# Performance work log

Hardware: AMD Instinct MI355X
Metric: run time of the kernel (lower is better)

## Reference

```python
import jax, jax.numpy as jnp
import numpy as np

B, T, D, S, P, R = 8, 512, 256, 64, 1024, 12


def setup_inputs() -> dict:
    key = jax.random.key(0)
    ks = jax.random.split(key, 8)
    encoded = jax.random.normal(ks[0], (B, T, D), dtype=jnp.float32)
    span_starts = jax.random.randint(ks[1], (B, S), 0, 500).astype(jnp.int32)
    span_lens = jax.random.randint(ks[2], (B, S), 0, 12).astype(jnp.int32)  # end = start + len + 1 <= T
    pair_head = jax.random.randint(ks[3], (B, P), 0, S).astype(jnp.int32)
    pair_tail = jax.random.randint(ks[4], (B, P), 0, S).astype(jnp.int32)
    W_linear = (jax.random.normal(ks[5], (2 * D, R), dtype=jnp.float32) / np.sqrt(2 * D)).astype(jnp.float32)
    b_linear = jnp.zeros((R,), dtype=jnp.float32)
    W_bilinear = (jax.random.normal(ks[6], (R, D, D), dtype=jnp.float32) / D).astype(jnp.float32)
    return dict(encoded=encoded, W_linear=W_linear, b_linear=b_linear, W_bilinear=W_bilinear,
                span_starts=span_starts, span_lens=span_lens, pair_head=pair_head, pair_tail=pair_tail)


def reference(encoded, W_linear, b_linear, W_bilinear, span_starts, span_lens, pair_head, pair_tail):
    # --- ragged span max-pooling (self.pool = max over encoded[b, start:end]) ---
    span_ends = span_starts + span_lens + 1  # exclusive end, length >= 1
    pos = jnp.arange(T)  # [T]
    in_span = (pos[None, None, :] >= span_starts[:, :, None]) & (pos[None, None, :] < span_ends[:, :, None])  # [B,S,T]
    neg_inf = jnp.finfo(encoded.dtype).min
    span_pooled = jnp.max(jnp.where(in_span[..., None], encoded[:, None, :, :], neg_inf), axis=2)  # [B,S,D]

    # --- pair feature gather: [span_pooled[head], span_pooled[tail]] ---
    head = jnp.take_along_axis(span_pooled, pair_head[..., None].astype(jnp.int32), axis=1)  # [B,P,D]
    tail = jnp.take_along_axis(span_pooled, pair_tail[..., None].astype(jnp.int32), axis=1)  # [B,P,D]
    pair_rep = jnp.concatenate([head, tail], axis=-1)  # [B,P,2D]

    # --- linear + bilinear classifier, sigmoid scores ---
    scores = pair_rep @ W_linear + b_linear  # [B,P,R]
    scores = scores + jnp.einsum('bpd,rde,bpe->bpr', head, W_bilinear, tail)
    return jax.nn.sigmoid(scores)
```

## Files before the change

### kernel.cpp

```cpp
#include <hip/hip_runtime.h>
#include <math.h>

#define B 8
#define T 512
#define D 256
#define S 64
#define P 1024
#define R 12

typedef __attribute__((ext_vector_type(8)))  short bf16x8;
typedef __attribute__((ext_vector_type(16))) float f32x16;

static __device__ inline short f2bf(float f) {
    union { float f; unsigned u; } v; v.f = f;
    unsigned u = v.u + 0x7fff + ((v.u >> 16) & 1);
    return (short)(u >> 16);
}
static __device__ inline float bf2f(unsigned short h) {
    union { unsigned u; float f; } v; v.u = ((unsigned)h) << 16;
    return v.f;
}

__global__ __launch_bounds__(256) void k_prep(
    const float* __restrict__ enc, const int* __restrict__ starts,
    const int* __restrict__ lens, const float* __restrict__ Wl,
    const float* __restrict__ Wb,
    float* __restrict__ sp, short* __restrict__ spb, float* __restrict__ lin,
    short* __restrict__ Wt)
{
    if (blockIdx.x < B * S) {
        int bs = blockIdx.x;
        int b  = bs >> 6;
        int d  = threadIdx.x;
        int st = starts[bs];
        int ln = lens[bs];

        const float* base = enc + ((size_t)(b * T + st)) * D + d;
        float m = base[0];
        #pragma unroll
        for (int i = 1; i < 12; ++i) {
            int idx = (i <= ln) ? i : ln;
            m = fmaxf(m, base[(size_t)idx * D]);
        }
        sp [(size_t)bs * D + d] = m;
        spb[(size_t)bs * D + d] = f2bf(m);

        __shared__ float smem[256];
        smem[d] = m;
        __syncthreads();

        int wave = d >> 6, lane = d & 63;
        #pragma unroll
        for (int oo = 0; oo < 6; ++oo) {
            int o = wave * 6 + oo;
            int r = (o < 12) ? o : (o - 12);
            int rowbase = (o < 12) ? 0 : D;
            float p = 0.f;
            #pragma unroll
            for (int k = 0; k < 4; ++k) {
                int dd = lane + 64 * k;
                p = fmaf(smem[dd], Wl[(size_t)(rowbase + dd) * R + r], p);
            }
            #pragma unroll
            for (int off = 32; off > 0; off >>= 1) p += __shfl_down(p, off, 64);
            if (lane == 0) lin[(size_t)bs * 24 + o] = p;
        }
    } else {
        int bid  = blockIdx.x - B * S;
        int dblk = bid & 31;
        int r    = bid >> 5;
        int e    = threadIdx.x;

        const float* src = Wb + ((size_t)r * D + dblk * 8) * D + e;
        short v[8];
        #pragma unroll
        for (int j = 0; j < 8; ++j) v[j] = f2bf(src[(size_t)j * D]);

        short* dst = Wt + ((size_t)r * D + e) * D + dblk * 8;
        *(bf16x8*)dst = *(bf16x8*)v;
    }
}

__global__ __launch_bounds__(256) void k_bilinear_mfma(
    const short* __restrict__ spb, const short* __restrict__ Wt,
    short* __restrict__ U)
{
    int wave = threadIdx.x >> 6;
    int lane = threadIdx.x & 63;
    int m0 = blockIdx.x * 64 + (wave >> 1) * 32;
    int n0 = blockIdx.y * 64 + (wave & 1) * 32;
    int r  = blockIdx.z;

    int half = lane >> 5;
    int mn   = lane & 31;

    const short* ap = spb + (size_t)(m0 + mn) * D + half * 8;
    const short* bp = Wt + ((size_t)r * D + (n0 + mn)) * D + half * 8;

    f32x16 acc = {};
    #pragma unroll
    for (int ks = 0; ks < 16; ++ks) {
        bf16x8 a = *(const bf16x8*)(ap + ks * 16);
        bf16x8 b = *(const bf16x8*)(bp + ks * 16);
        acc = __builtin_amdgcn_mfma_f32_32x32x16_bf16(a, b, acc, 0, 0, 0);
    }

    #pragma unroll
    for (int reg = 0; reg < 16; ++reg) {
        int m = m0 + (reg & 3) + 8 * (reg >> 2) + 4 * half;
        int n = n0 + mn;
        U[((size_t)m * R + r) * D + n] = f2bf(acc[reg]);
    }
}

__global__ __launch_bounds__(256) void k_scores(
    const float* __restrict__ sp, const short* __restrict__ U,
    const float* __restrict__ lin, const int* __restrict__ ph,
    const int* __restrict__ pt, const float* __restrict__ bl,
    float* __restrict__ out)
{
    int pair = blockIdx.x * 4 + (threadIdx.x >> 6);
    int lane = threadIdx.x & 63;
    int b = pair >> 10;
    int p = pair & 1023;

    int h = ph[(size_t)b * P + p];
    int t = pt[(size_t)b * P + p];

    float4 tv = ((const float4*)(sp + ((size_t)(b * S + t)) * D))[lane];
    const ushort4* Up = (const ushort4*)(U + ((size_t)(b * S + h)) * R * D);

    float acc[R];
    #pragma unroll
    for (int r = 0; r < R; ++r) {
        ushort4 u = Up[r * 64 + lane];
        float a = bf2f(u.x) * tv.x;
        a = fmaf(bf2f(u.y), tv.y, a);
        a = fmaf(bf2f(u.z), tv.z, a);
        a = fmaf(bf2f(u.w), tv.w, a);
        acc[r] = a;
    }
    #pragma unroll
    for (int off = 32; off > 0; off >>= 1) {
        #pragma unroll
        for (int r = 0; r < R; ++r) acc[r] += __shfl_down(acc[r], off, 64);
    }

    if (lane == 0) {
        const float* linH = lin + ((size_t)(b * S + h)) * 24;
        const float* linT = lin + ((size_t)(b * S + t)) * 24;
        float s[R];
        #pragma unroll
        for (int r = 0; r < R; ++r) {
            float sc = acc[r] + linH[r] + linT[12 + r] + bl[r];
            s[r] = 1.f / (1.f + expf(-sc));
        }
        float4* op = (float4*)(out + (size_t)(b * P + p) * R);
        op[0] = make_float4(s[0], s[1], s[2],  s[3]);
        op[1] = make_float4(s[4], s[5], s[6],  s[7]);
        op[2] = make_float4(s[8], s[9], s[10], s[11]);
    }
}

extern "C" void kernel_launch(void* const* d_in, const int* in_sizes, int n_in,
                              void* d_out, int out_size, void* d_ws, size_t ws_size,
                              hipStream_t stream) {
    const float* enc    = (const float*)d_in[0];
    const float* Wl     = (const float*)d_in[1];
    const float* bl     = (const float*)d_in[2];
    const float* Wb     = (const float*)d_in[3];
    const int*   starts = (const int*)d_in[4];
    const int*   lens   = (const int*)d_in[5];
    const int*   ph     = (const int*)d_in[6];
    const int*   pt     = (const int*)d_in[7];
    float* out = (float*)d_out;

    float* sp  = (float*)d_ws;
    float* lin = sp + (size_t)B * S * D;
    short* spb = (short*)(lin + (size_t)B * S * 24);
    short* U   = spb + (size_t)B * S * D;
    short* Wt  = U + (size_t)B * S * R * D;

    k_prep         <<<B * S + 32 * R, 256, 0, stream>>>(enc, starts, lens, Wl, Wb, sp, spb, lin, Wt);
    k_bilinear_mfma<<<dim3(8, 4, R),  256, 0, stream>>>(spb, Wt, U);
    k_scores       <<<B * P / 4,      256, 0, stream>>>(sp, U, lin, ph, pt, bl, out);
}
```

Measured before the change: 97.03 us.

## Precompute all span-pair bilinear scores with two chained MFMA GEMMs, then gather

Since S=64 spans per batch and P=1024 pairs, the bilinear term is computed for all 64x64 span pairs per batch and relation as V = (spans·W_r)·spansᵀ. Both GEMMs run in one block, with the intermediate kept in LDS. The score kernel becomes a per-pair gather of 12 floats plus the linear terms and sigmoid, replacing the per-pair 256-wide dot product with wave reductions. The second GEMM now uses bf16 tail features instead of fp32, which slightly reduces accuracy. Only 96 blocks run the GEMM stage, so GPU occupancy is low.

```diff
diff --git a/kernel.cpp b/kernel.cpp
--- a/kernel.cpp
+++ b/kernel.cpp
@@ -16,17 +16,12 @@
     unsigned u = v.u + 0x7fff + ((v.u >> 16) & 1);
     return (short)(u >> 16);
 }
-static __device__ inline float bf2f(unsigned short h) {
-    union { unsigned u; float f; } v; v.u = ((unsigned)h) << 16;
-    return v.f;
-}
 
 __global__ __launch_bounds__(256) void k_prep(
     const float* __restrict__ enc, const int* __restrict__ starts,
     const int* __restrict__ lens, const float* __restrict__ Wl,
     const float* __restrict__ Wb,
-    float* __restrict__ sp, short* __restrict__ spb, float* __restrict__ lin,
-    short* __restrict__ Wt)
+    short* __restrict__ spb, float* __restrict__ lin, short* __restrict__ Wt)
 {
     if (blockIdx.x < B * S) {
         int bs = blockIdx.x;
@@ -42,7 +37,6 @@
             int idx = (i <= ln) ? i : ln;
             m = fmaxf(m, base[(size_t)idx * D]);
         }
-        sp [(size_t)bs * D + d] = m;
         spb[(size_t)bs * D + d] = f2bf(m);
 
         __shared__ float smem[256];
@@ -81,84 +75,102 @@
     }
 }
 
-__global__ __launch_bounds__(256) void k_bilinear_mfma(
+#define LDSTRIDE 264
+__global__ __launch_bounds__(256) void k_bilinear_v(
     const short* __restrict__ spb, const short* __restrict__ Wt,
-    short* __restrict__ U)
+    float* __restrict__ V)
 {
+    int b = blockIdx.x;
+    int r = blockIdx.y;
     int wave = threadIdx.x >> 6;
     int lane = threadIdx.x & 63;
-    int m0 = blockIdx.x * 64 + (wave >> 1) * 32;
-    int n0 = blockIdx.y * 64 + (wave & 1) * 32;
-    int r  = blockIdx.z;
-
     int half = lane >> 5;
     int mn   = lane & 31;
 
-    const short* ap = spb + (size_t)(m0 + mn) * D + half * 8;
-    const short* bp = Wt + ((size_t)r * D + (n0 + mn)) * D + half * 8;
+    __shared__ short ldsU[64 * LDSTRIDE];
 
-    f32x16 acc = {};
-    #pragma unroll
-    for (int ks = 0; ks < 16; ++ks) {
-        bf16x8 a = *(const bf16x8*)(ap + ks * 16);
-        bf16x8 b = *(const bf16x8*)(bp + ks * 16);
-        acc = __builtin_amdgcn_mfma_f32_32x32x16_bf16(a, b, acc, 0, 0, 0);
+    {
+        int n0 = wave * 64;
+        const short* ap0 = spb + ((size_t)(b * 64 + mn))      * D + half * 8;
+        const short* ap1 = ap0 + 32 * D;
+        const short* bp0 = Wt + ((size_t)r * D + (n0 + mn))      * D + half * 8;
+        const short* bp1 = bp0 + 32 * D;
+
+        f32x16 acc00 = {}, acc01 = {}, acc10 = {}, acc11 = {};
+        #pragma unroll
+        for (int ks = 0; ks < 16; ++ks) {
+            bf16x8 a0 = *(const bf16x8*)(ap0 + ks * 16);
+            bf16x8 a1 = *(const bf16x8*)(ap1 + ks * 16);
+            bf16x8 b0 = *(const bf16x8*)(bp0 + ks * 16);
+            bf16x8 b1 = *(const bf16x8*)(bp1 + ks * 16);
+            acc00 = __builtin_amdgcn_mfma_f32_32x32x16_bf16(a0, b0, acc00, 0, 0, 0);
+            acc01 = __builtin_amdgcn_mfma_f32_32x32x16_bf16(a0, b1, acc01, 0, 0, 0);
+            acc10 = __builtin_amdgcn_mfma_f32_32x32x16_bf16(a1, b0, acc10, 0, 0, 0);
+            acc11 = __builtin_amdgcn_mfma_f32_32x32x16_bf16(a1, b1, acc11, 0, 0, 0);
+        }
+
+        #pragma unroll
+        for (int reg = 0; reg < 16; ++reg) {
+            int mrow = (reg & 3) + 8 * (reg >> 2) + 4 * half;
+            int e0 = n0 + mn, e1 = n0 + 32 + mn;
+            ldsU[(size_t)(mrow)      * LDSTRIDE + e0] = f2bf(acc00[reg]);
+            ldsU[(size_t)(mrow)      * LDSTRIDE + e1] = f2bf(acc01[reg]);
+            ldsU[(size_t)(mrow + 32) * LDSTRIDE + e0] = f2bf(acc10[reg]);
+            ldsU[(size_t)(mrow + 32) * LDSTRIDE + e1] = f2bf(acc11[reg]);
+        }
     }
+    __syncthreads();
 
-    #pragma unroll
-    for (int reg = 0; reg < 16; ++reg) {
-        int m = m0 + (reg & 3) + 8 * (reg >> 2) + 4 * half;
-        int n = n0 + mn;
-        U[((size_t)m * R + r) * D + n] = f2bf(acc[reg]);
+    {
+        int mt = (wave >> 1) * 32;
+        int nt = (wave & 1) * 32;
+        const short* ap = ldsU + (size_t)(mt + mn) * LDSTRIDE + half * 8;
+        const short* bp = spb + ((size_t)(b * 64 + nt + mn)) * D + half * 8;
+
+        f32x16 acc = {};
+        #pragma unroll
+        for (int ks = 0; ks < 16; ++ks) {
+            bf16x8 a = *(const bf16x8*)(ap + ks * 16);
+            bf16x8 bb = *(const bf16x8*)(bp + ks * 16);
+            acc = __builtin_amdgcn_mfma_f32_32x32x16_bf16(a, bb, acc, 0, 0, 0);
+        }
+
+        #pragma unroll
+        for (int reg = 0; reg < 16; ++reg) {
+            int s = mt + (reg & 3) + 8 * (reg >> 2) + 4 * half;
+            int t = nt + mn;
+            V[((size_t)((b * 64 + s) * 64 + t)) * R + r] = acc[reg];
+        }
     }
 }
 
-__global__ __launch_bounds__(256) void k_scores(
-    const float* __restrict__ sp, const short* __restrict__ U,
-    const float* __restrict__ lin, const int* __restrict__ ph,
-    const int* __restrict__ pt, const float* __restrict__ bl,
-    float* __restrict__ out)
+__global__ __launch_bounds__(256) void k_gather(
+    const float* __restrict__ V, const float* __restrict__ lin,
+    const int* __restrict__ ph, const int* __restrict__ pt,
+    const float* __restrict__ bl, float* __restrict__ out)
 {
-    int pair = blockIdx.x * 4 + (threadIdx.x >> 6);
-    int lane = threadIdx.x & 63;
+    int pair = blockIdx.x * 256 + threadIdx.x;
     int b = pair >> 10;
     int p = pair & 1023;
 
     int h = ph[(size_t)b * P + p];
     int t = pt[(size_t)b * P + p];
 
-    float4 tv = ((const float4*)(sp + ((size_t)(b * S + t)) * D))[lane];
-    const ushort4* Up = (const ushort4*)(U + ((size_t)(b * S + h)) * R * D);
+    const float4* vp = (const float4*)(V + ((size_t)((b * 64 + h) * 64 + t)) * R);
+    const float4* lH = (const float4*)(lin + (size_t)(b * 64 + h) * 24);
+    const float4* lT = (const float4*)(lin + (size_t)(b * 64 + t) * 24 + 12);
+    const float4* blv = (const float4*)bl;
 
-    float acc[R];
+    float4* op = (float4*)(out + (size_t)pair * R);
     #pragma unroll
-    for (int r = 0; r < R; ++r) {
-        ushort4 u = Up[r * 64 + lane];
-        float a = bf2f(u.x) * tv.x;
-        a = fmaf(bf2f(u.y), tv.y, a);
-        a = fmaf(bf2f(u.z), tv.z, a);
-        a = fmaf(bf2f(u.w), tv.w, a);
-        acc[r] = a;
-    }
-    #pragma unroll
-    for (int off = 32; off > 0; off >>= 1) {
-        #pragma unroll
-        for (int r = 0; r < R; ++r) acc[r] += __shfl_down(acc[r], off, 64);
-    }
-
-    if (lane == 0) {
-        const float* linH = lin + ((size_t)(b * S + h)) * 24;
-        const float* linT = lin + ((size_t)(b * S + t)) * 24;
-        float s[R];
-        #pragma unroll
-        for (int r = 0; r < R; ++r) {
-            float sc = acc[r] + linH[r] + linT[12 + r] + bl[r];
-            s[r] = 1.f / (1.f + expf(-sc));
-        }
-        float4* op = (float4*)(out + (size_t)(b * P + p) * R);
-        op[0] = make_float4(s[0], s[1], s[2],  s[3]);
-        op[1] = make_float4(s[4], s[5], s[6],  s[7]);
-        op[2] = make_float4(s[8], s[9], s[10], s[11]);
+    for (int q = 0; q < 3; ++q) {
+        float4 v = vp[q], a = lH[q], c = lT[q], d = blv[q];
+        float4 s;
+        s.x = 1.f / (1.f + expf(-(v.x + a.x + c.x + d.x)));
+        s.y = 1.f / (1.f + expf(-(v.y + a.y + c.y + d.y)));
+        s.z = 1.f / (1.f + expf(-(v.z + a.z + c.z + d.z)));
+        s.w = 1.f / (1.f + expf(-(v.w + a.w + c.w + d.w)));
+        op[q] = s;
     }
 }
 
@@ -175,13 +187,12 @@
     const int*   pt     = (const int*)d_in[7];
     float* out = (float*)d_out;
 
-    float* sp  = (float*)d_ws;
-    float* lin = sp + (size_t)B * S * D;
+    float* lin = (float*)d_ws;
     short* spb = (short*)(lin + (size_t)B * S * 24);
-    short* U   = spb + (size_t)B * S * D;
-    short* Wt  = U + (size_t)B * S * R * D;
+    short* Wt  = spb + (size_t)B * S * D;
+    float* V   = (float*)(Wt + (size_t)R * D * D);
 
-    k_prep         <<<B * S + 32 * R, 256, 0, stream>>>(enc, starts, lens, Wl, Wb, sp, spb, lin, Wt);
-    k_bilinear_mfma<<<dim3(8, 4, R),  256, 0, stream>>>(spb, Wt, U);
-    k_scores       <<<B * P / 4,      256, 0, stream>>>(sp, U, lin, ph, pt, bl, out);
+    k_prep      <<<B * S + 32 * R, 256, 0, stream>>>(enc, starts, lens, Wl, Wb, spb, lin, Wt);
+    k_bilinear_v<<<dim3(B, R),     256, 0, stream>>>(spb, Wt, V);
+    k_gather    <<<B * P / 256,    256, 0, stream>>>(V, lin, ph, pt, bl, out);
 }
```

Result: faster. 91.30 us (-5.9%).
